# Performance work log

Measured on AMD Instinct MI355X. Metric: run time of the kernel, lower is better.

## Reference

```python
import jax, jax.numpy as jnp
import numpy as np

N_NODES = 50000
N_EDGES = 1600000
IN_DIM = 128
OUT_DIM = 16
N_HEADS = 8


def setup_inputs() -> dict:
    key = jax.random.key(0)
    ks = jax.random.split(key, 9)
    s = 1.0 / np.sqrt(IN_DIM)
    return {
        "h": jax.random.normal(ks[0], (N_NODES, IN_DIM), jnp.float32),
        "Wq": jax.random.normal(ks[1], (IN_DIM, OUT_DIM * N_HEADS), jnp.float32) * s,
        "bq": jax.random.normal(ks[2], (OUT_DIM * N_HEADS,), jnp.float32) * 0.01,
        "Wk": jax.random.normal(ks[3], (IN_DIM, OUT_DIM * N_HEADS), jnp.float32) * s,
        "bk": jax.random.normal(ks[4], (OUT_DIM * N_HEADS,), jnp.float32) * 0.01,
        "Wv": jax.random.normal(ks[5], (IN_DIM, OUT_DIM * N_HEADS), jnp.float32) * s,
        "bv": jax.random.normal(ks[6], (OUT_DIM * N_HEADS,), jnp.float32) * 0.01,
        "src": jax.random.randint(ks[7], (N_EDGES,), 0, N_NODES, jnp.int32),
        "dst": jax.random.randint(ks[8], (N_EDGES,), 0, N_NODES, jnp.int32),
    }


def reference(h, Wq, bq, Wk, bk, Wv, bv, src, dst):
    n_nodes = h.shape[0]
    # node-wise Q/K/V projections -> [N, H, D]
    Q = (h @ Wq + bq).reshape(n_nodes, N_HEADS, OUT_DIM)
    K = (h @ Wk + bk).reshape(n_nodes, N_HEADS, OUT_DIM)
    V = (h @ Wv + bv).reshape(n_nodes, N_HEADS, OUT_DIM)
    # edge-wise score: (K[src] * Q[dst]).sum(-1), scaled-exp with clamp
    score = jnp.sum(K[src] * Q[dst], axis=-1)  # [E, H]
    score = jnp.exp(jnp.clip(score / np.sqrt(OUT_DIM), -5.0, 5.0))
    # scatter-sum weighted values and normalizers to dst nodes
    msg = V[src] * score[:, :, None]  # [E, H, D]
    wV = jax.ops.segment_sum(msg, dst, num_segments=n_nodes)  # [N, H, D]
    z = jax.ops.segment_sum(score, dst, num_segments=n_nodes)  # [N, H]
    return wV / (z[:, :, None] + 1e-6)
```

## Files before the change

### kernel.cpp

```cpp
#include <hip/hip_runtime.h>
#include <hip/hip_bf16.h>
#include <cstddef>

#define N_NODES 50000
#define N_EDGES 1600000
#define IN_DIM 128
#define OUT_DIM 16
#define N_HEADS 8
#define QKV_DIM 128
#define HS_STRIDE 136

#define SUBB 3125
#define SUBB_PAD 3136
#define BCAP 1024
#define BH_CHUNK 16384
#define BH_BLOCKS 98

typedef __hip_bfloat16 bf16;
typedef short bf16x8 __attribute__((ext_vector_type(8)));
typedef float f32x4  __attribute__((ext_vector_type(4)));

__device__ __forceinline__ float b2f(bf16 x) { return __bfloat162float(x); }

__device__ __forceinline__ float u16tof(unsigned int u) {
    unsigned int x = u << 16;
    float f;
    __builtin_memcpy(&f, &x, 4);
    return f;
}

__device__ __forceinline__ unsigned short f2bf(float v) {
    bf16 b = __float2bfloat16(v);
    unsigned short u;
    __builtin_memcpy(&u, &b, 2);
    return u;
}

__global__ __launch_bounds__(256) void init_kernel(int* __restrict__ p, int n) {
    int i = blockIdx.x * 256 + threadIdx.x;
    if (i < n) p[i] = 0;
}

__global__ __launch_bounds__(256) void detect_kernel(const unsigned short* __restrict__ hraw,
                                                     int* __restrict__ flag) {
    int t = threadIdx.x;
    int cnt = 0;
    for (int i = t; i < 8192; i += 256) {
        unsigned short u = hraw[i];
        int e = (u >> 7) & 0xFF;
        if (e == 0xFF || e > 0x85 || (e == 0 && (u & 0x7F) != 0)) cnt++;
    }
    atomicAdd(flag, cnt);
}

__global__ __launch_bounds__(256) void sentinel_kernel(unsigned short* __restrict__ out, int n) {
    int i = blockIdx.x * 256 + threadIdx.x;
    if (i < n) out[i] = 0x42C8;
}

__global__ __launch_bounds__(256) void prep_kernel(
    const void* __restrict__ Wqr, const void* __restrict__ bqr,
    const void* __restrict__ Wkr, const void* __restrict__ bkr,
    const void* __restrict__ Wvr, const void* __restrict__ bvr,
    const int* __restrict__ flag,
    unsigned short* __restrict__ Wfrag, float* __restrict__ bias_f)
{
    const bool f32 = (*flag > 100);
    int tid = blockIdx.x * 256 + threadIdx.x;

    if (tid < 384) {
        int mat = tid >> 7, c = tid & 127;
        const void* bp = (mat == 0) ? bqr : (mat == 1) ? bkr : bvr;
        bias_f[tid] = f32 ? ((const float*)bp)[c] : b2f(((const bf16*)bp)[c]);
    }
    if (tid >= 6144) return;

    int l  = tid & 63;
    int s  = (tid >> 6) & 3;
    int nt = tid >> 8;
    int n  = nt * 16 + (l & 15);
    int k0 = s * 32 + (l >> 4) * 8;
    int mat = n >> 7, c = n & 127;
    const void* Wp = (mat == 0) ? Wqr : (mat == 1) ? Wkr : Wvr;

    unsigned short v[8];
#pragma unroll
    for (int j = 0; j < 8; ++j) {
        int k = k0 + j;
        float w = f32 ? ((const float*)Wp)[k * QKV_DIM + c]
                      : b2f(((const bf16*)Wp)[k * QKV_DIM + c]);
        v[j] = f2bf(w);
    }
    ushort4* o = (ushort4*)(Wfrag + (size_t)tid * 8);
    o[0] = make_ushort4(v[0], v[1], v[2], v[3]);
    o[1] = make_ushort4(v[4], v[5], v[6], v[7]);
}

__global__ __launch_bounds__(256) void gemm_kernel(
    const void* __restrict__ hraw,
    const unsigned short* __restrict__ Wfrag, const float* __restrict__ bias_f,
    const int* __restrict__ flag,
    unsigned short* __restrict__ Qt, unsigned short* __restrict__ KVt)
{
    __shared__ __align__(16) unsigned short hs[64 * HS_STRIDE];

    const bool f32 = (*flag > 100);
    const int m0  = blockIdx.x * 64;
    const int tid = threadIdx.x;

#pragma unroll
    for (int it = 0; it < 8; ++it) {
        int idx = it * 1024 + tid * 4;
        int r = idx >> 7, k = idx & 127;
        int row = m0 + r;
        ushort4 w4 = make_ushort4(0, 0, 0, 0);
        if (row < N_NODES) {
            if (f32) {
                float4 v4 = ((const float4*)hraw)[(size_t)row * 32 + (k >> 2)];
                w4 = make_ushort4(f2bf(v4.x), f2bf(v4.y), f2bf(v4.z), f2bf(v4.w));
            } else {
                uint2 u = ((const uint2*)hraw)[(size_t)row * 32 + (k >> 2)];
                w4 = make_ushort4((unsigned short)(u.x & 0xffffu), (unsigned short)(u.x >> 16),
                                  (unsigned short)(u.y & 0xffffu), (unsigned short)(u.y >> 16));
            }
        }
        *(ushort4*)&hs[r * HS_STRIDE + k] = w4;
    }
    __syncthreads();

    const int lane = tid & 63;
    const int wave = tid >> 6;
    const int qd   = lane >> 4;
    const int ln15 = lane & 15;

    bf16x8 afr[4][4];
#pragma unroll
    for (int ms = 0; ms < 4; ++ms)
#pragma unroll
        for (int s = 0; s < 4; ++s)
            afr[ms][s] = *(const bf16x8*)&hs[(ms * 16 + ln15) * HS_STRIDE + s * 32 + qd * 8];

#pragma unroll
    for (int i = 0; i < 6; ++i) {
        const int nt  = wave + i * 4;
        const int col = nt * 16 + ln15;
        const float bs = bias_f[col];
        const int mat = col >> 7, c127 = col & 127;
        const int coff = (mat == 0) ? c127
                       : 4 * (c127 >> 1) + (c127 & 1) + ((mat == 2) ? 2 : 0);

        bf16x8 bfr[4];
#pragma unroll
        for (int s = 0; s < 4; ++s)
            bfr[s] = *(const bf16x8*)(Wfrag + ((size_t)(nt * 4 + s) * 64 + lane) * 8);

#pragma unroll
        for (int ms = 0; ms < 4; ++ms) {
            f32x4 acc = {0.f, 0.f, 0.f, 0.f};
#pragma unroll
            for (int s = 0; s < 4; ++s)
                acc = __builtin_amdgcn_mfma_f32_16x16x32_bf16(afr[ms][s], bfr[s], acc, 0, 0, 0);
#pragma unroll
            for (int r = 0; r < 4; ++r) {
                int row = m0 + ms * 16 + qd * 4 + r;
                if (row < N_NODES) {
                    unsigned short val = f2bf(acc[r] + bs);
                    if (mat == 0) Qt[row * 128 + coff] = val;
                    else          KVt[row * 256 + coff] = val;
                }
            }
        }
    }
}

__global__ __launch_bounds__(256) void scatter_kernel(const int* __restrict__ src,
                                                      const int* __restrict__ dst,
                                                      int* __restrict__ gcursor,
                                                      unsigned int* __restrict__ packed) {
    __shared__ int lcnt[SUBB];
    __shared__ int lbase[SUBB];
    int t = threadIdx.x;
    for (int i = t; i < SUBB; i += 256) lcnt[i] = 0;
    __syncthreads();
    int base = blockIdx.x * BH_CHUNK;
    for (int i = 0; i < 64; ++i) {
        int e = base + i * 256 + t;
        if (e < N_EDGES) atomicAdd(&lcnt[dst[e] >> 4], 1);
    }
    __syncthreads();
    for (int i = t; i < SUBB; i += 256) {
        int c = lcnt[i];
        lbase[i] = c ? atomicAdd(&gcursor[i], c) : 0;
        lcnt[i] = 0;
    }
    __syncthreads();
    for (int i = 0; i < 64; ++i) {
        int e = base + i * 256 + t;
        if (e < N_EDGES) {
            int d = dst[e];
            int b = d >> 4;
            int pos = lbase[b] + atomicAdd(&lcnt[b], 1);
            if (pos < BCAP)
                packed[b * BCAP + pos] = (unsigned int)src[e] | ((unsigned int)(d & 15) << 16);
        }
    }
}

__global__ __launch_bounds__(256) void bucket_agg_kernel(
    const unsigned short* __restrict__ Qt, const unsigned short* __restrict__ KVt,
    const unsigned int* __restrict__ packed, const int* __restrict__ gcursor,
    const int* __restrict__ flag, void* __restrict__ out)
{
    __shared__ unsigned int   lds_pk[BCAP];
    __shared__ unsigned short lds_src[BCAP];
    __shared__ int cnt16[16], base16[16], cur16[16];

    const int sb = blockIdx.x;
    const int t  = threadIdx.x;
    const int nb = min(gcursor[sb], BCAP);

    if (t < 16) { cnt16[t] = 0; cur16[t] = 0; }
    __syncthreads();

    for (int j = t; j < nb; j += 256) {
        unsigned int pk = packed[sb * BCAP + j];
        lds_pk[j] = pk;
        atomicAdd(&cnt16[(pk >> 16) & 15], 1);
    }
    __syncthreads();
    if (t == 0) {
        int acc = 0;
#pragma unroll
        for (int i = 0; i < 16; ++i) { base16[i] = acc; acc += cnt16[i]; }
    }
    __syncthreads();
    for (int j = t; j < nb; j += 256) {
        unsigned int pk = lds_pk[j];
        int dl = (pk >> 16) & 15;
        int pos = base16[dl] + atomicAdd(&cur16[dl], 1);
        lds_src[pos] = (unsigned short)(pk & 0xffffu);
    }
    __syncthreads();

    const int wave = t >> 6;
    const int lane = t & 63;
    const uint2* KV2 = (const uint2*)KVt;
    const bool of32 = (*flag > 100);

    for (int dl = wave; dl < 16; dl += 4) {
        const int d = sb * 16 + dl;
        unsigned int qu = ((const unsigned int*)Qt)[d * 64 + lane];
        const float q0 = u16tof(qu & 0xffffu), q1 = u16tof(qu >> 16);
        const int off = base16[dl];
        const int n   = cnt16[dl];

        float a0 = 0.f, a1 = 0.f, zz = 0.f;

        int j = 0;
        for (; j + 8 <= n; j += 8) {
            int s[8];
#pragma unroll
            for (int u = 0; u < 8; ++u) s[u] = lds_src[off + j + u];
            uint2 kv[8];
#pragma unroll
            for (int u = 0; u < 8; ++u) kv[u] = KV2[s[u] * 64 + lane];
#pragma unroll
            for (int u = 0; u < 8; ++u) {
                float p = u16tof(kv[u].x & 0xffffu) * q0 + u16tof(kv[u].x >> 16) * q1;
                p += __shfl_xor(p, 1);
                p += __shfl_xor(p, 2);
                p += __shfl_xor(p, 4);
                float sc = __expf(__builtin_amdgcn_fmed3f(p * 0.25f, -5.f, 5.f));
                a0 = fmaf(u16tof(kv[u].y & 0xffffu), sc, a0);
                a1 = fmaf(u16tof(kv[u].y >> 16),     sc, a1);
                zz += sc;
            }
        }
        if (j + 4 <= n) {
            int s[4];
#pragma unroll
            for (int u = 0; u < 4; ++u) s[u] = lds_src[off + j + u];
            uint2 kv[4];
#pragma unroll
            for (int u = 0; u < 4; ++u) kv[u] = KV2[s[u] * 64 + lane];
#pragma unroll
            for (int u = 0; u < 4; ++u) {
                float p = u16tof(kv[u].x & 0xffffu) * q0 + u16tof(kv[u].x >> 16) * q1;
                p += __shfl_xor(p, 1);
                p += __shfl_xor(p, 2);
                p += __shfl_xor(p, 4);
                float sc = __expf(__builtin_amdgcn_fmed3f(p * 0.25f, -5.f, 5.f));
                a0 = fmaf(u16tof(kv[u].y & 0xffffu), sc, a0);
                a1 = fmaf(u16tof(kv[u].y >> 16),     sc, a1);
                zz += sc;
            }
            j += 4;
        }
        for (; j < n; ++j) {
            int s = lds_src[off + j];
            uint2 kv = KV2[s * 64 + lane];
            float p = u16tof(kv.x & 0xffffu) * q0 + u16tof(kv.x >> 16) * q1;
            p += __shfl_xor(p, 1);
            p += __shfl_xor(p, 2);
            p += __shfl_xor(p, 4);
            float sc = __expf(__builtin_amdgcn_fmed3f(p * 0.25f, -5.f, 5.f));
            a0 = fmaf(u16tof(kv.y & 0xffffu), sc, a0);
            a1 = fmaf(u16tof(kv.y >> 16),     sc, a1);
            zz += sc;
        }

        const float r0 = a0 / (zz + 1e-6f);
        const float r1 = a1 / (zz + 1e-6f);

        if (of32) {
            ((float2*)((float*)out + (size_t)d * QKV_DIM))[lane] = make_float2(r0, r1);
        } else {
            __hip_bfloat162 pk2;
            pk2.x = __float2bfloat16(r0);
            pk2.y = __float2bfloat16(r1);
            ((__hip_bfloat162*)out)[d * 64 + lane] = pk2;
        }
    }
}

extern "C" void kernel_launch(void* const* d_in, const int* in_sizes, int n_in,
                              void* d_out, int out_size, void* d_ws, size_t ws_size,
                              hipStream_t stream)
{
    const void* h  = d_in[0];
    const void* Wq = d_in[1];
    const void* bq = d_in[2];
    const void* Wk = d_in[3];
    const void* bk = d_in[4];
    const void* Wv = d_in[5];
    const void* bv = d_in[6];
    const int*  src = (const int*)d_in[7];
    const int*  dst = (const int*)d_in[8];

    const size_t NQ = (size_t)N_NODES * QKV_DIM;
    const size_t WFRAG_N = 24 * 4 * 64 * 8;

    const size_t need = 3 * NQ * 2 + WFRAG_N * 2 + 384 * 4
                      + ((size_t)SUBB_PAD + 16) * sizeof(int)
                      + (size_t)SUBB * BCAP * 4;

    if (ws_size < need) {
        sentinel_kernel<<<(out_size + 255) / 256, 256, 0, stream>>>((unsigned short*)d_out, out_size);
        return;
    }

    unsigned short* Qt  = (unsigned short*)d_ws;
    unsigned short* KVt = Qt + NQ;
    unsigned short* Wfrag = KVt + 2 * NQ;
    float* bias_f = (float*)(Wfrag + WFRAG_N);
    int* gcursor = (int*)(bias_f + 384);
    int* flag    = gcursor + SUBB_PAD;
    unsigned int* packed = (unsigned int*)(flag + 16);

    const int zero_n = SUBB_PAD + 16;
    init_kernel<<<(zero_n + 255) / 256, 256, 0, stream>>>(gcursor, zero_n);
    detect_kernel<<<1, 256, 0, stream>>>((const unsigned short*)h, flag);

    prep_kernel<<<24, 256, 0, stream>>>(Wq, bq, Wk, bk, Wv, bv, flag, Wfrag, bias_f);

    const int gemm_blocks = (N_NODES + 63) / 64;
    gemm_kernel<<<gemm_blocks, 256, 0, stream>>>(h, Wfrag, bias_f, flag, Qt, KVt);

    scatter_kernel<<<BH_BLOCKS, 256, 0, stream>>>(src, dst, gcursor, packed);

    bucket_agg_kernel<<<SUBB, 256, 0, stream>>>(Qt, KVt, packed, gcursor, flag, d_out);
}
```

Measured before the change: 302.9 us.

## Process two edges per wave with 16-byte K/V gathers and 4 dims per lane

The interleaved K/V layout written by the projection kernel changes from 2-wide to 4-wide groups, so each lane can load a uint4 holding 4 K and 4 V values. Each half-wave (32 lanes) now handles a different edge, so a wave processes two edges per step. This halves the shuffle depth per score and doubles bytes per load instruction. Partial sums are combined with a cross-half shuffle at the end, and the odd tail edge is masked for the upper half. The cost is more registers and an extra final reduction.

```diff
diff --git a/kernel.cpp b/kernel.cpp
--- a/kernel.cpp
+++ b/kernel.cpp
@@ -147,7 +147,7 @@
         const float bs = bias_f[col];
         const int mat = col >> 7, c127 = col & 127;
         const int coff = (mat == 0) ? c127
-                       : 4 * (c127 >> 1) + (c127 & 1) + ((mat == 2) ? 2 : 0);
+                       : 8 * (c127 >> 2) + (c127 & 3) + ((mat == 2) ? 4 : 0);
 
         bf16x8 bfr[4];
 #pragma unroll
@@ -244,81 +244,78 @@
 
     const int wave = t >> 6;
     const int lane = t & 63;
-    const uint2* KV2 = (const uint2*)KVt;
+    const int half = lane >> 5;
+    const int hl   = lane & 31;
+    const uint4* KV4 = (const uint4*)KVt;
     const bool of32 = (*flag > 100);
 
     for (int dl = wave; dl < 16; dl += 4) {
         const int d = sb * 16 + dl;
-        unsigned int qu = ((const unsigned int*)Qt)[d * 64 + lane];
-        const float q0 = u16tof(qu & 0xffffu), q1 = u16tof(qu >> 16);
+        uint2 qw = ((const uint2*)Qt)[d * 32 + hl];
+        const float q0 = u16tof(qw.x & 0xffffu), q1 = u16tof(qw.x >> 16);
+        const float q2 = u16tof(qw.y & 0xffffu), q3 = u16tof(qw.y >> 16);
         const int off = base16[dl];
         const int n   = cnt16[dl];
 
-        float a0 = 0.f, a1 = 0.f, zz = 0.f;
+        float a0 = 0.f, a1 = 0.f, a2 = 0.f, a3 = 0.f, zz = 0.f;
+
+#define CONSUME(KV, SCMASK)                                                     \
+        {                                                                       \
+            float p = fmaf(u16tof((KV).x & 0xffffu), q0,                        \
+                      fmaf(u16tof((KV).x >> 16), q1,                            \
+                      fmaf(u16tof((KV).y & 0xffffu), q2,                        \
+                           u16tof((KV).y >> 16) * q3)));                        \
+            p += __shfl_xor(p, 1);                                              \
+            p += __shfl_xor(p, 2);                                              \
+            float sc = __expf(__builtin_amdgcn_fmed3f(p * 0.25f, -5.f, 5.f));   \
+            sc *= (SCMASK);                                                     \
+            a0 = fmaf(u16tof((KV).z & 0xffffu), sc, a0);                        \
+            a1 = fmaf(u16tof((KV).z >> 16),     sc, a1);                        \
+            a2 = fmaf(u16tof((KV).w & 0xffffu), sc, a2);                        \
+            a3 = fmaf(u16tof((KV).w >> 16),     sc, a3);                        \
+            zz += sc;                                                           \
+        }
 
         int j = 0;
         for (; j + 8 <= n; j += 8) {
-            int s[8];
-#pragma unroll
-            for (int u = 0; u < 8; ++u) s[u] = lds_src[off + j + u];
-            uint2 kv[8];
-#pragma unroll
-            for (int u = 0; u < 8; ++u) kv[u] = KV2[s[u] * 64 + lane];
-#pragma unroll
-            for (int u = 0; u < 8; ++u) {
-                float p = u16tof(kv[u].x & 0xffffu) * q0 + u16tof(kv[u].x >> 16) * q1;
-                p += __shfl_xor(p, 1);
-                p += __shfl_xor(p, 2);
-                p += __shfl_xor(p, 4);
-                float sc = __expf(__builtin_amdgcn_fmed3f(p * 0.25f, -5.f, 5.f));
-                a0 = fmaf(u16tof(kv[u].y & 0xffffu), sc, a0);
-                a1 = fmaf(u16tof(kv[u].y >> 16),     sc, a1);
-                zz += sc;
+            int e[4];
+#pragma unroll
+            for (int u = 0; u < 4; ++u) e[u] = lds_src[off + j + 2 * u + half];
+            uint4 kv[4];
+#pragma unroll
+            for (int u = 0; u < 4; ++u) kv[u] = KV4[e[u] * 32 + hl];
+#pragma unroll
+            for (int u = 0; u < 4; ++u) CONSUME(kv[u], 1.f)
+        }
+        for (; j + 2 <= n; j += 2) {
+            int e = lds_src[off + j + half];
+            uint4 kv = KV4[e * 32 + hl];
+            CONSUME(kv, 1.f)
+        }
+        if (j < n) {
+            int e = lds_src[off + j];
+            uint4 kv = KV4[e * 32 + hl];
+            CONSUME(kv, (half == 0) ? 1.f : 0.f)
+        }
+#undef CONSUME
+
+        a0 += __shfl_xor(a0, 32);
+        a1 += __shfl_xor(a1, 32);
+        a2 += __shfl_xor(a2, 32);
+        a3 += __shfl_xor(a3, 32);
+        zz += __shfl_xor(zz, 32);
+
+        const float inv = 1.f / (zz + 1e-6f);
+        const float r0 = a0 * inv, r1 = a1 * inv, r2 = a2 * inv, r3 = a3 * inv;
+
+        if (half == 0) {
+            if (of32) {
+                ((float4*)out)[d * 32 + hl] = make_float4(r0, r1, r2, r3);
+            } else {
+                unsigned int w0 = ((unsigned int)f2bf(r1) << 16) | f2bf(r0);
+                unsigned int w1 = ((unsigned int)f2bf(r3) << 16) | f2bf(r2);
+                ((uint2*)out)[d * 32 + hl] = make_uint2(w0, w1);
             }
-        }
-        if (j + 4 <= n) {
-            int s[4];
-#pragma unroll
-            for (int u = 0; u < 4; ++u) s[u] = lds_src[off + j + u];
-            uint2 kv[4];
-#pragma unroll
-            for (int u = 0; u < 4; ++u) kv[u] = KV2[s[u] * 64 + lane];
-#pragma unroll
-            for (int u = 0; u < 4; ++u) {
-                float p = u16tof(kv[u].x & 0xffffu) * q0 + u16tof(kv[u].x >> 16) * q1;
-                p += __shfl_xor(p, 1);
-                p += __shfl_xor(p, 2);
-                p += __shfl_xor(p, 4);
-                float sc = __expf(__builtin_amdgcn_fmed3f(p * 0.25f, -5.f, 5.f));
-                a0 = fmaf(u16tof(kv[u].y & 0xffffu), sc, a0);
-                a1 = fmaf(u16tof(kv[u].y >> 16),     sc, a1);
-                zz += sc;
-            }
-            j += 4;
-        }
-        for (; j < n; ++j) {
-            int s = lds_src[off + j];
-            uint2 kv = KV2[s * 64 + lane];
-            float p = u16tof(kv.x & 0xffffu) * q0 + u16tof(kv.x >> 16) * q1;
-            p += __shfl_xor(p, 1);
-            p += __shfl_xor(p, 2);
-            p += __shfl_xor(p, 4);
-            float sc = __expf(__builtin_amdgcn_fmed3f(p * 0.25f, -5.f, 5.f));
-            a0 = fmaf(u16tof(kv.y & 0xffffu), sc, a0);
-            a1 = fmaf(u16tof(kv.y >> 16),     sc, a1);
-            zz += sc;
-        }
-
-        const float r0 = a0 / (zz + 1e-6f);
-        const float r1 = a1 / (zz + 1e-6f);
-
-        if (of32) {
-            ((float2*)((float*)out + (size_t)d * QKV_DIM))[lane] = make_float2(r0, r1);
-        } else {
-            __hip_bfloat162 pk2;
-            pk2.x = __float2bfloat16(r0);
-            pk2.y = __float2bfloat16(r1);
-            ((__hip_bfloat162*)out)[d * 64 + lane] = pk2;
         }
     }
 }
```

After: 309.1 us. 2.1% more time.
